# Performance work log

Hardware: AMD Instinct MI355X
Metric: run time of the kernel (lower is better)

## Reference

```python
import jax, jax.numpy as jnp
import numpy as np

B, D, H, W = 1024, 256, 8, 8
NS, ITERS, HID = 8, 5, 256  # HID = max(dim, 128)
EPS = 1e-8


def _ln(x, w, b, axes):
    mu = x.mean(axes, keepdims=True)
    var = x.var(axes, keepdims=True)
    return (x - mu) * jax.lax.rsqrt(var + 1e-5) * w + b


def _grid():
    ranges = [np.linspace(0.0, 1.0, num=r) for r in (H, W)]
    g = np.stack(np.meshgrid(*ranges, indexing='ij'), -1).reshape(H, W, -1)[None].astype(np.float32)
    return jnp.asarray(np.concatenate([g, 1.0 - g], -1))  # [1,H,W,4]


def setup_inputs():
    key = jax.random.key(0)
    ks = jax.random.split(key, 16)
    r = lambda i, shape, s=0.02: jax.random.normal(ks[i], shape, jnp.float32) * s
    d = D
    return {
        'inputs': jax.random.normal(ks[0], (B, D, H, W), jnp.float32),
        'slots_noise': jax.random.normal(ks[1], (B, NS, D), jnp.float32),
        'pos_W': r(2, (4, d)), 'pos_b': jnp.zeros((d,), jnp.float32),
        'enln_w': jnp.ones((H * W, d), jnp.float32), 'enln_b': jnp.zeros((H * W, d), jnp.float32),
        'f1W': r(3, (d, d)), 'f1b': jnp.zeros((d,), jnp.float32),
        'f2W': r(4, (d, d)), 'f2b': jnp.zeros((d,), jnp.float32),
        'ni_w': jnp.ones((d,), jnp.float32), 'ni_b': jnp.zeros((d,), jnp.float32),
        'qW': r(5, (d, d)), 'qb': jnp.zeros((d,), jnp.float32),
        'kW': r(6, (d, d)), 'kb': jnp.zeros((d,), jnp.float32),
        'vW': r(7, (d, d)), 'vb': jnp.zeros((d,), jnp.float32),
        'gih': r(8, (3 * d, d)), 'ghh': r(9, (3 * d, d)),
        'bih': jnp.zeros((3 * d,), jnp.float32), 'bhh': jnp.zeros((3 * d,), jnp.float32),
        'ns_w': jnp.ones((d,), jnp.float32), 'ns_b': jnp.zeros((d,), jnp.float32),
        'pf_w': jnp.ones((d,), jnp.float32), 'pf_b': jnp.zeros((d,), jnp.float32),
        'm1W': r(10, (d, HID)), 'm1b': jnp.zeros((HID,), jnp.float32),
        'm2W': r(11, (HID, d)), 'm2b': jnp.zeros((d,), jnp.float32),
        'slots_mu': r(12, (1, 1, d), 0.1),
        'slots_sigma': r(13, (1, 1, d), 0.1),
    }


def reference(inputs, slots_noise, pos_W, pos_b, enln_w, enln_b, f1W, f1b, f2W, f2b,
              ni_w, ni_b, qW, qb, kW, kb, vW, vb, gih, ghh, bih, bhh,
              ns_w, ns_b, pf_w, pf_b, m1W, m1b, m2W, m2b, slots_mu, slots_sigma):
    b, d = inputs.shape[0], inputs.shape[1]
    scale = d ** -0.5
    # encoder_transformation (position=True)
    x = jnp.transpose(inputs, (0, 2, 3, 1))          # [B,H,W,D]
    x = x + (_grid() @ pos_W + pos_b)                # SoftPositionEmbed
    x = x.reshape(b, H * W, d)                       # flatten spatial -> tokens
    x = _ln(x, enln_w, enln_b, (-2, -1))             # LayerNorm([ntokens, dim])
    x = jax.nn.relu(x @ f1W + f1b)
    x = jax.nn.relu(x @ f2W + f2b)
    x = _ln(x, ni_w, ni_b, (-1,))                    # norm_input
    k = x @ kW + kb                                  # [B,N,D]
    v = x @ vW + vb
    # slot init: torch.normal(mu, exp(0.5*sigma)) with explicit noise
    slots = slots_mu + jnp.exp(0.5 * slots_sigma) * slots_noise  # [B,S,D]
    for _ in range(ITERS):
        slots_prev = slots
        q = _ln(slots, ns_w, ns_b, (-1,)) @ qW + qb
        dots = jnp.einsum('bid,bjd->bij', q, k) * scale  # [B,S,N]
        attn = jax.nn.softmax(dots, axis=1) + EPS        # softmax over SLOT axis
        attn = attn / attn.sum(-1, keepdims=True)        # renormalize over tokens
        updates = jnp.einsum('bjd,bij->bid', v, attn)    # [B,S,D]
        # GRUCell(updates, slots_prev)
        gx = updates @ gih.T + bih
        gh = slots_prev @ ghh.T + bhh
        xr, xz, xn = jnp.split(gx, 3, -1)
        hr, hz, hn = jnp.split(gh, 3, -1)
        r_ = jax.nn.sigmoid(xr + hr)
        z_ = jax.nn.sigmoid(xz + hz)
        n_ = jnp.tanh(xn + r_ * hn)
        slots = (1.0 - z_) * n_ + z_ * slots_prev
        # residual MLP
        h = jax.nn.relu(_ln(slots, pf_w, pf_b, (-1,)) @ m1W + m1b)
        slots = slots + (h @ m2W + m2b)
    return slots
```

## Files before the change

kernel.cpp:

```cpp
#include <hip/hip_runtime.h>
#include <math.h>


typedef __attribute__((ext_vector_type(8))) short short8;
typedef __attribute__((ext_vector_type(4))) float f32x4;
typedef unsigned long long ull;

__device__ __forceinline__ unsigned short f2bf(float f) {
    union { float f; unsigned u; } x; x.f = f;
    unsigned r = x.u + 0x7fffu + ((x.u >> 16) & 1u);
    return (unsigned short)(r >> 16);
}
__device__ __forceinline__ float bf2f(unsigned short h) {
    union { unsigned u; float f; } x; x.u = ((unsigned)h) << 16;
    return x.f;
}
__device__ __forceinline__ float sigmoidf_(float x) { return 1.f / (1.f + expf(-x)); }
__device__ __forceinline__ ull pack4(float a, float b, float c, float d) {
    return (ull)f2bf(a) | ((ull)f2bf(b) << 16) | ((ull)f2bf(c) << 32) | ((ull)f2bf(d) << 48);
}
__device__ __forceinline__ short8 afrag256(const unsigned short* buf, int row, int k) {
    return *(const short8*)(buf + row * 256 + (k ^ ((row & 7) << 3)));
}
__device__ __forceinline__ short8 afrag64(const unsigned short* buf, int row, int k) {
// ... 201 lines not shown
                XL[lrow * 256 + ((wc + 16 + lr) ^ ((lrow & 7) << 3))] = f2bf(fmaxf(acc[mt][1][r] + b1, 0.f));
            }
    }
    __syncthreads();

    {
        const float4 w4 = *(const float4*)(niw + lane * 4);
        const float4 b4 = *(const float4*)(nib + lane * 4);
        for (int rr = 0; rr < 8; ++rr) {
            int row = wave * 8 + rr;
            ull* p = (ull*)(XL + row * 256 + ((lane * 4) ^ ((row & 7) << 3)));
            ull pk = *p;
            float v0 = bf2f((unsigned short)pk),         v1 = bf2f((unsigned short)(pk >> 16));
            float v2 = bf2f((unsigned short)(pk >> 32)), v3 = bf2f((unsigned short)(pk >> 48));
            float s1 = v0 + v1 + v2 + v3;
            float s2 = v0 * v0 + v1 * v1 + v2 * v2 + v3 * v3;
            #pragma unroll
            for (int m = 32; m >= 1; m >>= 1) { s1 += __shfl_xor(s1, m); s2 += __shfl_xor(s2, m); }
            float mu_ = s1 * (1.f / 256.f);
            float rs_ = rsqrtf(s2 * (1.f / 256.f) - mu_ * mu_ + 1e-5f);
            *p = pack4((v0 - mu_) * rs_ * w4.x + b4.x, (v1 - mu_) * rs_ * w4.y + b4.y,
                       (v2 - mu_) * rs_ * w4.z + b4.z, (v3 - mu_) * rs_ * w4.w + b4.w);
        }
    }
    __syncthreads();

    {
        short8 w0[8], w1[8];
        const unsigned short* wp0 = kt + (size_t)(wc + lr) * 256 + lk;
        const unsigned short* wp1 = kt + (size_t)(wc + 16 + lr) * 256 + lk;
        #pragma unroll
        for (int kk = 0; kk < 8; ++kk) {
            w0[kk] = *(const short8*)(wp0 + kk * 32);
            w1[kk] = *(const short8*)(wp1 + kk * 32);
        }
        const float b0 = kb[wc + lr], b1 = kb[wc + 16 + lr];
        for (int mt = 0; mt < 4; ++mt) {
            short8 a[8];
            #pragma unroll
            for (int kk = 0; kk < 8; ++kk) a[kk] = afrag256(XL, mt * 16 + lr, kk * 32 + lk);
            f32x4 a0 = (f32x4){0.f,0.f,0.f,0.f}, a1 = (f32x4){0.f,0.f,0.f,0.f};
            #pragma unroll
            for (int kk = 0; kk < 8; ++kk) {
                a0 = __builtin_amdgcn_mfma_f32_16x16x32_bf16(a[kk], w0[kk], a0, 0, 0, 0);
                a1 = __builtin_amdgcn_mfma_f32_16x16x32_bf16(a[kk], w1[kk], a1, 0, 0, 0);
            }
            #pragma unroll
            for (int r = 0; r < 4; ++r) {
                size_t row = (size_t)b * 64 + mt * 16 + mr + r;
                ks[row * 256 + wc + lr]      = f2bf(a0[r] + b0);
                ks[row * 256 + wc + 16 + lr] = f2bf(a1[r] + b1);
            }
        }
    }
    {
        short8 w0[8], w1[8];
        const unsigned short* wp0 = vwt + (size_t)(wc + lr) * 256 + lk;
        const unsigned short* wp1 = vwt + (size_t)(wc + 16 + lr) * 256 + lk;
        #pragma unroll
        for (int kk = 0; kk < 8; ++kk) {
            w0[kk] = *(const short8*)(wp0 + kk * 32);
            w1[kk] = *(const short8*)(wp1 + kk * 32);
        }
        const float b0 = vb[wc + lr], b1 = vb[wc + 16 + lr];
        for (int mt = 0; mt < 4; ++mt) {
            short8 a[8];
            #pragma unroll
            for (int kk = 0; kk < 8; ++kk) a[kk] = afrag256(XL, mt * 16 + lr, kk * 32 + lk);
            f32x4 a0 = (f32x4){0.f,0.f,0.f,0.f}, a1 = (f32x4){0.f,0.f,0.f,0.f};
            #pragma unroll
            for (int kk = 0; kk < 8; ++kk) {
                a0 = __builtin_amdgcn_mfma_f32_16x16x32_bf16(a[kk], w0[kk], a0, 0, 0, 0);
                a1 = __builtin_amdgcn_mfma_f32_16x16x32_bf16(a[kk], w1[kk], a1, 0, 0, 0);
            }
            int t0 = mt * 16 + mr;
            *(ull*)(vt + (size_t)b * 16384 + (size_t)(wc + lr) * 64 + t0) =
                pack4(a0[0] + b0, a0[1] + b0, a0[2] + b0, a0[3] + b0);
            *(ull*)(vt + (size_t)b * 16384 + (size_t)(wc + 16 + lr) * 64 + t0) =
                pack4(a1[0] + b1, a1[1] + b1, a1[2] + b1, a1[3] + b1);
        }
    }
}

__launch_bounds__(512)
__global__ void iter_kernel(
    const unsigned short* __restrict__ Kb, const unsigned short* __restrict__ Vtb,
    const unsigned short* __restrict__ qt,
    const unsigned short* __restrict__ gihb, const unsigned short* __restrict__ ghhb,
    const unsigned short* __restrict__ m1t,  const unsigned short* __restrict__ m2t,
    const float* __restrict__ qb,  const float* __restrict__ bih, const float* __restrict__ bhh,
    const float* __restrict__ pfw, const float* __restrict__ pfb,
    const float* __restrict__ m1b, const float* __restrict__ m2b,
    const float* __restrict__ nsw, const float* __restrict__ nsb,
    float* __restrict__ ping, unsigned short* __restrict__ sraw,
    unsigned short* __restrict__ lnq,
    float* __restrict__ outf, int last)
{
    __shared__ unsigned short SA[32 * 256];
    __shared__ unsigned short SS[32 * 256];
    __shared__ unsigned short QP[4][16 * 256];
    __shared__ unsigned short AT[4][16 * 64];
    __shared__ unsigned short US[32 * 256];
    __shared__ float AF[4][8][72];
    __shared__ float HL[32][256];

    const int t = threadIdx.x, lane = t & 63, wave = t >> 6;
    const int m0 = blockIdx.x * 32;
    const int b0 = blockIdx.x * 4;
    const int lr = lane & 15, lk = (lane >> 4) * 8, mr = (lane >> 4) * 4;
    const int wc = wave * 32;

    for (int i = 0; i < 4; ++i) {
        int id = t + 512 * i;
        int row = id >> 6, c4 = (id & 63) * 4;
        size_t g = ((size_t)m0 + row) * 256 + c4;
        int sw = c4 ^ ((row & 7) << 3);
        *(ull*)(SA + row * 256 + sw) = *(const ull*)(lnq + g);
        *(ull*)(SS + row * 256 + sw) = *(const ull*)(sraw + g);
    }
    for (int i = t; i < 2048; i += 512) {
        int bb = i >> 9, rem = i & 511;
        int row = 8 + (rem >> 6), c4 = (rem & 63) * 4;
        *(ull*)(&QP[bb][row * 256 + c4]) = 0;
    }
    for (int i = t; i < 1024; i += 512) ((ull*)AT)[i] = 0;
    __syncthreads();

    {
        short8 w0[8], w1[8];
        const unsigned short* wp0 = qt + (size_t)(wc + lr) * 256 + lk;
        const unsigned short* wp1 = qt + (size_t)(wc + 16 + lr) * 256 + lk;
        #pragma unroll
        for (int kk = 0; kk < 8; ++kk) {
            w0[kk] = *(const short8*)(wp0 + kk * 32);
            w1[kk] = *(const short8*)(wp1 + kk * 32);
        }
        const float bq0 = qb[wc + lr], bq1 = qb[wc + 16 + lr];
        #pragma unroll
        for (int mt = 0; mt < 2; ++mt) {
            short8 a[8];
            #pragma unroll
            for (int kk = 0; kk < 8; ++kk) a[kk] = afrag256(SA, mt * 16 + lr, kk * 32 + lk);
            f32x4 a0 = (f32x4){0.f,0.f,0.f,0.f}, a1 = (f32x4){0.f,0.f,0.f,0.f};
            #pragma unroll
            for (int kk = 0; kk < 8; ++kk) {
                a0 = __builtin_amdgcn_mfma_f32_16x16x32_bf16(a[kk], w0[kk], a0, 0, 0, 0);
                a1 = __builtin_amdgcn_mfma_f32_16x16x32_bf16(a[kk], w1[kk], a1, 0, 0, 0);
            }
            #pragma unroll
            for (int r = 0; r < 4; ++r) {
                int row = mt * 16 + mr + r;
                int bb = row >> 3, sr = row & 7;
                QP[bb][sr * 256 + ((wc + lr)      ^ (sr << 3))] = f2bf(a0[r] + bq0);
                QP[bb][sr * 256 + ((wc + 16 + lr) ^ (sr << 3))] = f2bf(a1[r] + bq1);
            }
        }
    }
    __syncthreads();

    {
        const int bb = wave >> 1, th = wave & 1;
        const int b = b0 + bb;
        short8 af[8];
        #pragma unroll
        for (int kk = 0; kk < 8; ++kk) af[kk] = afrag256(QP[bb], lr, kk * 32 + lk);
        #pragma unroll
        for (int tf = 0; tf < 2; ++tf) {
            int n0 = th * 32 + tf * 16;
            f32x4 acc = (f32x4){0.f,0.f,0.f,0.f};
            const unsigned short* kp = Kb + ((size_t)b * 64 + n0 + lr) * 256 + lk;
            #pragma unroll
            for (int kk = 0; kk < 8; ++kk)
                acc = __builtin_amdgcn_mfma_f32_16x16x32_bf16(af[kk], *(const short8*)(kp + kk * 32), acc, 0, 0, 0);
            #pragma unroll
            for (int r = 0; r < 4; ++r)
                if (mr + r < 8) AF[bb][mr + r][n0 + lr] = acc[r] * 0.0625f;
        }
    }
    __syncthreads();

    if (t < 256) {
        int b2 = t >> 6, tok = t & 63;
        float mx = AF[b2][0][tok];
        #pragma unroll
        for (int s = 1; s < 8; ++s) mx = fmaxf(mx, AF[b2][s][tok]);
        float e[8], den = 0.f;
        #pragma unroll
        for (int s = 0; s < 8; ++s) { e[s] = expf(AF[b2][s][tok] - mx); den += e[s]; }
        float inv = 1.f / den;
        #pragma unroll
        for (int s = 0; s < 8; ++s) AF[b2][s][tok] = e[s] * inv + 1e-8f;
    }
    __syncthreads();

    #pragma unroll
    for (int j = 0; j < 4; ++j) {
        int row = wave * 4 + j;
        int bb = row >> 3, sr = row & 7;
        float v = AF[bb][sr][lane];
        float ssum = v;
        #pragma unroll
        for (int m = 32; m >= 1; m >>= 1) ssum += __shfl_xor(ssum, m);
        AT[bb][sr * 64 + (lane ^ (sr << 3))] = f2bf(v / ssum);
    }
    __syncthreads();

    {
        const int bb = wave >> 1, ch = wave & 1;
        const int b = b0 + bb;
        short8 a0 = afrag64(AT[bb], lr, lk);
        short8 a1 = afrag64(AT[bb], lr, 32 + lk);
        #pragma unroll
        for (int cf = 0; cf < 8; ++cf) {
            int col = ch * 128 + cf * 16 + lr;
            const unsigned short* vp = Vtb + (size_t)b * 16384 + (size_t)col * 64;
            f32x4 acc = (f32x4){0.f,0.f,0.f,0.f};
            acc = __builtin_amdgcn_mfma_f32_16x16x32_bf16(a0, *(const short8*)(vp + lk), acc, 0, 0, 0);
            acc = __builtin_amdgcn_mfma_f32_16x16x32_bf16(a1, *(const short8*)(vp + 32 + lk), acc, 0, 0, 0);
            #pragma unroll
            for (int r = 0; r < 4; ++r)
                if (mr + r < 8) {
                    int row = bb * 8 + mr + r;
                    US[row * 256 + (col ^ ((row & 7) << 3))] = f2bf(acc[r]);
                }
        }
    }
    __syncthreads();

    {
        f32x4 aR[2][2], aZ[2][2], aN[2][2], aH[2][2];
        #pragma unroll
        for (int cf = 0; cf < 2; ++cf)
            #pragma unroll
            for (int m = 0; m < 2; ++m) {
                aR[cf][m] = (f32x4){0.f,0.f,0.f,0.f}; aZ[cf][m] = (f32x4){0.f,0.f,0.f,0.f};
                aN[cf][m] = (f32x4){0.f,0.f,0.f,0.f}; aH[cf][m] = (f32x4){0.f,0.f,0.f,0.f};
            }
        #pragma unroll
        for (int g = 0; g < 3; ++g) {
            #pragma unroll
            for (int cf = 0; cf < 2; ++cf) {
                int col = wc + cf * 16 + lr;
                const unsigned short* px = gihb + (size_t)(g * 256 + col) * 256 + lk;
                const unsigned short* ph = ghhb + (size_t)(g * 256 + col) * 256 + lk;
                short8 wx[8], wh[8];
                #pragma unroll
                for (int kk = 0; kk < 8; ++kk) {
                    wx[kk] = *(const short8*)(px + kk * 32);
                    wh[kk] = *(const short8*)(ph + kk * 32);
                }
                #pragma unroll
                for (int m = 0; m < 2; ++m) {
                    #pragma unroll
                    for (int kk = 0; kk < 8; ++kk) {
                        short8 u = afrag256(US, m * 16 + lr, kk * 32 + lk);
                        short8 s = afrag256(SS, m * 16 + lr, kk * 32 + lk);
                        if (g == 0) {
                            aR[cf][m] = __builtin_amdgcn_mfma_f32_16x16x32_bf16(u, wx[kk], aR[cf][m], 0, 0, 0);
                            aR[cf][m] = __builtin_amdgcn_mfma_f32_16x16x32_bf16(s, wh[kk], aR[cf][m], 0, 0, 0);
                        } else if (g == 1) {
                            aZ[cf][m] = __builtin_amdgcn_mfma_f32_16x16x32_bf16(u, wx[kk], aZ[cf][m], 0, 0, 0);
                            aZ[cf][m] = __builtin_amdgcn_mfma_f32_16x16x32_bf16(s, wh[kk], aZ[cf][m], 0, 0, 0);
                        } else {
                            aN[cf][m] = __builtin_amdgcn_mfma_f32_16x16x32_bf16(u, wx[kk], aN[cf][m], 0, 0, 0);
                            aH[cf][m] = __builtin_amdgcn_mfma_f32_16x16x32_bf16(s, wh[kk], aH[cf][m], 0, 0, 0);
                        }
                    }
                }
            }
        }
        #pragma unroll
        for (int cf = 0; cf < 2; ++cf) {
            int col = wc + cf * 16 + lr;
            float bR  = bih[col] + bhh[col];
            float bZ  = bih[col + 256] + bhh[col + 256];
            float bXN = bih[col + 512], bHN = bhh[col + 512];
            #pragma unroll
            for (int m = 0; m < 2; ++m)
                #pragma unroll
                for (int r = 0; r < 4; ++r) {
                    int row = m * 16 + mr + r;
                    float prev = ping[((size_t)m0 + row) * 256 + col];
                    float rr = sigmoidf_(aR[cf][m][r] + bR);
                    float zz = sigmoidf_(aZ[cf][m][r] + bZ);
                    float nn = tanhf(aN[cf][m][r] + bXN + rr * (aH[cf][m][r] + bHN));
                    HL[row][col] = (1.f - zz) * nn + zz * prev;
                }
        }
    }
    __syncthreads();
    {
        const float4 w4 = *(const float4*)(pfw + lane * 4);
        const float4 b4 = *(const float4*)(pfb + lane * 4);
        #pragma unroll
        for (int rr = 0; rr < 4; ++rr) {
            int row = wave * 4 + rr;
            float4 v = *(const float4*)&HL[row][lane * 4];
            float s1 = v.x + v.y + v.z + v.w;
            float s2 = v.x * v.x + v.y * v.y + v.z * v.z + v.w * v.w;
            #pragma unroll
            for (int m = 32; m >= 1; m >>= 1) { s1 += __shfl_xor(s1, m); s2 += __shfl_xor(s2, m); }
            float mu_ = s1 * (1.f / 256.f);
            float rs_ = rsqrtf(s2 * (1.f / 256.f) - mu_ * mu_ + 1e-5f);
            *(ull*)(SA + row * 256 + ((lane * 4) ^ ((row & 7) << 3))) = pack4(
                (v.x - mu_) * rs_ * w4.x + b4.x, (v.y - mu_) * rs_ * w4.y + b4.y,
                (v.z - mu_) * rs_ * w4.z + b4.z, (v.w - mu_) * rs_ * w4.w + b4.w);
        }
    }
    __syncthreads();

    {
        short8 w0[8], w1[8];
        const unsigned short* wp0 = m1t + (size_t)(wc + lr) * 256 + lk;
        const unsigned short* wp1 = m1t + (size_t)(wc + 16 + lr) * 256 + lk;
        #pragma unroll
        for (int kk = 0; kk < 8; ++kk) {
            w0[kk] = *(const short8*)(wp0 + kk * 32);
            w1[kk] = *(const short8*)(wp1 + kk * 32);
        }
        const float b0 = m1b[wc + lr], b1 = m1b[wc + 16 + lr];
        #pragma unroll
        for (int mt = 0; mt < 2; ++mt) {
            short8 a[8];
            #pragma unroll
            for (int kk = 0; kk < 8; ++kk) a[kk] = afrag256(SA, mt * 16 + lr, kk * 32 + lk);
            f32x4 a0 = (f32x4){0.f,0.f,0.f,0.f}, a1 = (f32x4){0.f,0.f,0.f,0.f};
            #pragma unroll
            for (int kk = 0; kk < 8; ++kk) {
                a0 = __builtin_amdgcn_mfma_f32_16x16x32_bf16(a[kk], w0[kk], a0, 0, 0, 0);
                a1 = __builtin_amdgcn_mfma_f32_16x16x32_bf16(a[kk], w1[kk], a1, 0, 0, 0);
            }
            #pragma unroll
            for (int r = 0; r < 4; ++r) {
                int row = mt * 16 + mr + r;
                US[row * 256 + ((wc + lr)      ^ ((row & 7) << 3))] = f2bf(fmaxf(a0[r] + b0, 0.f));
                US[row * 256 + ((wc + 16 + lr) ^ ((row & 7) << 3))] = f2bf(fmaxf(a1[r] + b1, 0.f));
            }
        }
    }
    __syncthreads();

    {
        short8 w0[8], w1[8];
        const unsigned short* wp0 = m2t + (size_t)(wc + lr) * 256 + lk;
        const unsigned short* wp1 = m2t + (size_t)(wc + 16 + lr) * 256 + lk;
        #pragma unroll
        for (int kk = 0; kk < 8; ++kk) {
            w0[kk] = *(const short8*)(wp0 + kk * 32);
            w1[kk] = *(const short8*)(wp1 + kk * 32);
        }
        const float b0 = m2b[wc + lr], b1 = m2b[wc + 16 + lr];
        #pragma unroll
        for (int mt = 0; mt < 2; ++mt) {
            short8 a[8];
            #pragma unroll
            for (int kk = 0; kk < 8; ++kk) a[kk] = afrag256(US, mt * 16 + lr, kk * 32 + lk);
            f32x4 a0 = (f32x4){0.f,0.f,0.f,0.f}, a1 = (f32x4){0.f,0.f,0.f,0.f};
            #pragma unroll
            for (int kk = 0; kk < 8; ++kk) {
                a0 = __builtin_amdgcn_mfma_f32_16x16x32_bf16(a[kk], w0[kk], a0, 0, 0, 0);
                a1 = __builtin_amdgcn_mfma_f32_16x16x32_bf16(a[kk], w1[kk], a1, 0, 0, 0);
            }
            #pragma unroll
            for (int r = 0; r < 4; ++r) {
                int row = mt * 16 + mr + r;
                HL[row][wc + lr]      = a0[r] + b0 + HL[row][wc + lr];
                HL[row][wc + 16 + lr] = a1[r] + b1 + HL[row][wc + 16 + lr];
            }
        }
    }
    __syncthreads();
    {
        const float4 w4 = *(const float4*)(nsw + lane * 4);
        const float4 b4 = *(const float4*)(nsb + lane * 4);
        #pragma unroll
        for (int rr = 0; rr < 4; ++rr) {
            int row = wave * 4 + rr;
            size_t off = ((size_t)m0 + row) * 256 + lane * 4;
            float4 v = *(const float4*)&HL[row][lane * 4];
            if (last) {
                *(float4*)(outf + off) = v;
            } else {
                float s1 = v.x + v.y + v.z + v.w;
                float s2 = v.x * v.x + v.y * v.y + v.z * v.z + v.w * v.w;
                #pragma unroll
                for (int m = 32; m >= 1; m >>= 1) { s1 += __shfl_xor(s1, m); s2 += __shfl_xor(s2, m); }
                float mu_ = s1 * (1.f / 256.f);
                float rs_ = rsqrtf(s2 * (1.f / 256.f) - mu_ * mu_ + 1e-5f);
                *(float4*)(ping + off) = v;
                *(ull*)(sraw + off) = pack4(v.x, v.y, v.z, v.w);
                *(ull*)(lnq + off) = pack4(
                    (v.x - mu_) * rs_ * w4.x + b4.x, (v.y - mu_) * rs_ * w4.y + b4.y,
                    (v.z - mu_) * rs_ * w4.z + b4.z, (v.w - mu_) * rs_ * w4.w + b4.w);
            }
        }
    }
}

extern "C" void kernel_launch(void* const* d_in, const int* in_sizes, int n_in,
                              void* d_out, int out_size, void* d_ws, size_t ws_size,
                              hipStream_t stream) {
    (void)in_sizes; (void)n_in; (void)ws_size; (void)out_size;
    unsigned short* wsb  = (unsigned short*)d_ws;
    unsigned short* bufB = wsb + (1u << 20);
    unsigned short* ksb  = bufB + 16777216;
    unsigned short* vtb  = ksb + 16777216;
    float* ping = (float*)(vtb + 16777216);
    unsigned short* srawb = (unsigned short*)(ping + 2097152);
    unsigned short* lnqb  = srawb + 2097152;

    const unsigned short* f1t  = wsb;
    const unsigned short* f2t  = wsb + 65536;
    const unsigned short* kt   = wsb + 131072;
    const unsigned short* vwt  = wsb + 196608;
    const unsigned short* qt   = wsb + 262144;
    const unsigned short* m1t  = wsb + 327680;
    const unsigned short* m2t  = wsb + 393216;
    const unsigned short* gihb = wsb + 458752;
    const unsigned short* ghhb = wsb + 655360;

    convert_weights<<<dim3(1664), dim3(512), 0, stream>>>(
        (const float*)d_in[6],  (const float*)d_in[8],  (const float*)d_in[14],
        (const float*)d_in[16], (const float*)d_in[12], (const float*)d_in[26],
        (const float*)d_in[28], (const float*)d_in[18], (const float*)d_in[19], wsb);

    enc1_kernel<<<dim3(1024), dim3(512), 0, stream>>>(
        (const float*)d_in[0], (const float*)d_in[2], (const float*)d_in[3],
        (const float*)d_in[4], (const float*)d_in[5],
        f1t, (const float*)d_in[7], bufB);

    enc2_kernel<<<dim3(1024), dim3(512), 0, stream>>>(
        bufB, f2t, (const float*)d_in[9],
        (const float*)d_in[10], (const float*)d_in[11],
        kt, (const float*)d_in[15], vwt, (const float*)d_in[17],
        ksb, vtb);

    slot_init<<<dim3(1024), dim3(512), 0, stream>>>(
        (const float*)d_in[30], (const float*)d_in[31], (const float*)d_in[1],
        (const float*)d_in[22], (const float*)d_in[23], ping, srawb, lnqb);

    for (int it = 0; it < 5; ++it) {
        iter_kernel<<<dim3(256), dim3(512), 0, stream>>>(
            ksb, vtb, qt, gihb, ghhb, m1t, m2t,
            (const float*)d_in[13], (const float*)d_in[20], (const float*)d_in[21],
            (const float*)d_in[24], (const float*)d_in[25],
            (const float*)d_in[27], (const float*)d_in[29],
            (const float*)d_in[22], (const float*)d_in[23],
            ping, srawb, lnqb,
            (float*)d_out, it == 4 ? 1 : 0);
    }
}
```

Before: 440.7 us.

## Double iter_kernel block size to 1024 threads, halving per-wave work

```diff
diff --git a/kernel.cpp b/kernel.cpp
--- a/kernel.cpp
+++ b/kernel.cpp
@@ -307,7 +307,7 @@
     }
 }
 
-__launch_bounds__(512)
+__launch_bounds__(1024)
 __global__ void iter_kernel(
     const unsigned short* __restrict__ Kb, const unsigned short* __restrict__ Vtb,
     const unsigned short* __restrict__ qt,
@@ -333,74 +333,64 @@
     const int m0 = blockIdx.x * 32;
     const int b0 = blockIdx.x * 4;
     const int lr = lane & 15, lk = (lane >> 4) * 8, mr = (lane >> 4) * 4;
-    const int wc = wave * 32;
-
-    for (int i = 0; i < 4; ++i) {
-        int id = t + 512 * i;
+    const int wc = wave * 16;
+
+    for (int i = 0; i < 2; ++i) {
+        int id = t + 1024 * i;
         int row = id >> 6, c4 = (id & 63) * 4;
         size_t g = ((size_t)m0 + row) * 256 + c4;
         int sw = c4 ^ ((row & 7) << 3);
         *(ull*)(SA + row * 256 + sw) = *(const ull*)(lnq + g);
         *(ull*)(SS + row * 256 + sw) = *(const ull*)(sraw + g);
     }
-    for (int i = t; i < 2048; i += 512) {
+    for (int i = t; i < 2048; i += 1024) {
         int bb = i >> 9, rem = i & 511;
         int row = 8 + (rem >> 6), c4 = (rem & 63) * 4;
         *(ull*)(&QP[bb][row * 256 + c4]) = 0;
     }
-    for (int i = t; i < 1024; i += 512) ((ull*)AT)[i] = 0;
-    __syncthreads();
-
-    {
-        short8 w0[8], w1[8];
+    if (t < 1024) ((ull*)AT)[t] = 0;
+    __syncthreads();
+
+    {
+        short8 w0[8];
         const unsigned short* wp0 = qt + (size_t)(wc + lr) * 256 + lk;
-        const unsigned short* wp1 = qt + (size_t)(wc + 16 + lr) * 256 + lk;
-        #pragma unroll
-        for (int kk = 0; kk < 8; ++kk) {
-            w0[kk] = *(const short8*)(wp0 + kk * 32);
-            w1[kk] = *(const short8*)(wp1 + kk * 32);
-        }
-        const float bq0 = qb[wc + lr], bq1 = qb[wc + 16 + lr];
+        #pragma unroll
+        for (int kk = 0; kk < 8; ++kk) w0[kk] = *(const short8*)(wp0 + kk * 32);
+        const float bq0 = qb[wc + lr];
         #pragma unroll
         for (int mt = 0; mt < 2; ++mt) {
             short8 a[8];
             #pragma unroll
             for (int kk = 0; kk < 8; ++kk) a[kk] = afrag256(SA, mt * 16 + lr, kk * 32 + lk);
-            f32x4 a0 = (f32x4){0.f,0.f,0.f,0.f}, a1 = (f32x4){0.f,0.f,0.f,0.f};
-            #pragma unroll
-            for (int kk = 0; kk < 8; ++kk) {
+            f32x4 a0 = (f32x4){0.f,0.f,0.f,0.f};
+            #pragma unroll
+            for (int kk = 0; kk < 8; ++kk)
                 a0 = __builtin_amdgcn_mfma_f32_16x16x32_bf16(a[kk], w0[kk], a0, 0, 0, 0);
-                a1 = __builtin_amdgcn_mfma_f32_16x16x32_bf16(a[kk], w1[kk], a1, 0, 0, 0);
-            }
             #pragma unroll
             for (int r = 0; r < 4; ++r) {
                 int row = mt * 16 + mr + r;
                 int bb = row >> 3, sr = row & 7;
-                QP[bb][sr * 256 + ((wc + lr)      ^ (sr << 3))] = f2bf(a0[r] + bq0);
-                QP[bb][sr * 256 + ((wc + 16 + lr) ^ (sr << 3))] = f2bf(a1[r] + bq1);
-            }
-        }
-    }
-    __syncthreads();
-
-    {
-        const int bb = wave >> 1, th = wave & 1;
+                QP[bb][sr * 256 + ((wc + lr) ^ (sr << 3))] = f2bf(a0[r] + bq0);
+            }
+        }
+    }
+    __syncthreads();
+
+    {
+        const int bb = wave >> 2, th = wave & 3;
         const int b = b0 + bb;
         short8 af[8];
         #pragma unroll
         for (int kk = 0; kk < 8; ++kk) af[kk] = afrag256(QP[bb], lr, kk * 32 + lk);
-        #pragma unroll
-        for (int tf = 0; tf < 2; ++tf) {
-            int n0 = th * 32 + tf * 16;
-            f32x4 acc = (f32x4){0.f,0.f,0.f,0.f};
-            const unsigned short* kp = Kb + ((size_t)b * 64 + n0 + lr) * 256 + lk;
-            #pragma unroll
-            for (int kk = 0; kk < 8; ++kk)
-                acc = __builtin_amdgcn_mfma_f32_16x16x32_bf16(af[kk], *(const short8*)(kp + kk * 32), acc, 0, 0, 0);
-            #pragma unroll
-            for (int r = 0; r < 4; ++r)
-                if (mr + r < 8) AF[bb][mr + r][n0 + lr] = acc[r] * 0.0625f;
-        }
+        int n0 = th * 16;
+        f32x4 acc = (f32x4){0.f,0.f,0.f,0.f};
+        const unsigned short* kp = Kb + ((size_t)b * 64 + n0 + lr) * 256 + lk;
+        #pragma unroll
+        for (int kk = 0; kk < 8; ++kk)
+            acc = __builtin_amdgcn_mfma_f32_16x16x32_bf16(af[kk], *(const short8*)(kp + kk * 32), acc, 0, 0, 0);
+        #pragma unroll
+        for (int r = 0; r < 4; ++r)
+            if (mr + r < 8) AF[bb][mr + r][n0 + lr] = acc[r] * 0.0625f;
     }
     __syncthreads();
 
@@ -419,8 +409,8 @@
     __syncthreads();
 
     #pragma unroll
-    for (int j = 0; j < 4; ++j) {
-        int row = wave * 4 + j;
+    for (int j = 0; j < 2; ++j) {
+        int row = wave * 2 + j;
         int bb = row >> 3, sr = row & 7;
         float v = AF[bb][sr][lane];
         float ssum = v;
@@ -431,13 +421,13 @@
     __syncthreads();
 
     {
-        const int bb = wave >> 1, ch = wave & 1;
+        const int bb = wave >> 2, ch = wave & 3;
         const int b = b0 + bb;
         short8 a0 = afrag64(AT[bb], lr, lk);
         short8 a1 = afrag64(AT[bb], lr, 32 + lk);
         #pragma unroll
-        for (int cf = 0; cf < 8; ++cf) {
-            int col = ch * 128 + cf * 16 + lr;
+        for (int cf = 0; cf < 4; ++cf) {
+            int col = ch * 64 + cf * 16 + lr;
             const unsigned short* vp = Vtb + (size_t)b * 16384 + (size_t)col * 64;
             f32x4 acc = (f32x4){0.f,0.f,0.f,0.f};
             acc = __builtin_amdgcn_mfma_f32_16x16x32_bf16(a0, *(const short8*)(vp + lk), acc, 0, 0, 0);
@@ -453,73 +443,64 @@
     __syncthreads();
 
     {
-        f32x4 aR[2][2], aZ[2][2], aN[2][2], aH[2][2];
-        #pragma unroll
-        for (int cf = 0; cf < 2; ++cf)
+        f32x4 aR[2], aZ[2], aN[2], aH[2];
+        #pragma unroll
+        for (int m = 0; m < 2; ++m) {
+            aR[m] = (f32x4){0.f,0.f,0.f,0.f}; aZ[m] = (f32x4){0.f,0.f,0.f,0.f};
+            aN[m] = (f32x4){0.f,0.f,0.f,0.f}; aH[m] = (f32x4){0.f,0.f,0.f,0.f};
+        }
+        const int col = wc + lr;
+        #pragma unroll
+        for (int g = 0; g < 3; ++g) {
+            const unsigned short* px = gihb + (size_t)(g * 256 + col) * 256 + lk;
+            const unsigned short* ph = ghhb + (size_t)(g * 256 + col) * 256 + lk;
+            short8 wx[8], wh[8];
+            #pragma unroll
+            for (int kk = 0; kk < 8; ++kk) {
+                wx[kk] = *(const short8*)(px + kk * 32);
+                wh[kk] = *(const short8*)(ph + kk * 32);
+            }
             #pragma unroll
             for (int m = 0; m < 2; ++m) {
-                aR[cf][m] = (f32x4){0.f,0.f,0.f,0.f}; aZ[cf][m] = (f32x4){0.f,0.f,0.f,0.f};
-                aN[cf][m] = (f32x4){0.f,0.f,0.f,0.f}; aH[cf][m] = (f32x4){0.f,0.f,0.f,0.f};
-            }
-        #pragma unroll
-        for (int g = 0; g < 3; ++g) {
-            #pragma unroll
-            for (int cf = 0; cf < 2; ++cf) {
-                int col = wc + cf * 16 + lr;
-                const unsigned short* px = gihb + (size_t)(g * 256 + col) * 256 + lk;
-                const unsigned short* ph = ghhb + (size_t)(g * 256 + col) * 256 + lk;
-                short8 wx[8], wh[8];
                 #pragma unroll
                 for (int kk = 0; kk < 8; ++kk) {
-                    wx[kk] = *(const short8*)(px + kk * 32);
-                    wh[kk] = *(const short8*)(ph + kk * 32);
-                }
-                #pragma unroll
-                for (int m = 0; m < 2; ++m) {
-                    #pragma unroll
-                    for (int kk = 0; kk < 8; ++kk) {
-                        short8 u = afrag256(US, m * 16 + lr, kk * 32 + lk);
-                        short8 s = afrag256(SS, m * 16 + lr, kk * 32 + lk);
-                        if (g == 0) {
-                            aR[cf][m] = __builtin_amdgcn_mfma_f32_16x16x32_bf16(u, wx[kk], aR[cf][m], 0, 0, 0);
-                            aR[cf][m] = __builtin_amdgcn_mfma_f32_16x16x32_bf16(s, wh[kk], aR[cf][m], 0, 0, 0);
-                        } else if (g == 1) {
-                            aZ[cf][m] = __builtin_amdgcn_mfma_f32_16x16x32_bf16(u, wx[kk], aZ[cf][m], 0, 0, 0);
-                            aZ[cf][m] = __builtin_amdgcn_mfma_f32_16x16x32_bf16(s, wh[kk], aZ[cf][m], 0, 0, 0);
-                        } else {
-                            aN[cf][m] = __builtin_amdgcn_mfma_f32_16x16x32_bf16(u, wx[kk], aN[cf][m], 0, 0, 0);
-                            aH[cf][m] = __builtin_amdgcn_mfma_f32_16x16x32_bf16(s, wh[kk], aH[cf][m], 0, 0, 0);
-                        }
+                    short8 u = afrag256(US, m * 16 + lr, kk * 32 + lk);
+                    short8 s = afrag256(SS, m * 16 + lr, kk * 32 + lk);
+                    if (g == 0) {
+                        aR[m] = __builtin_amdgcn_mfma_f32_16x16x32_bf16(u, wx[kk], aR[m], 0, 0, 0);
+                        aR[m] = __builtin_amdgcn_mfma_f32_16x16x32_bf16(s, wh[kk], aR[m], 0, 0, 0);
+                    } else if (g == 1) {
+                        aZ[m] = __builtin_amdgcn_mfma_f32_16x16x32_bf16(u, wx[kk], aZ[m], 0, 0, 0);
+                        aZ[m] = __builtin_amdgcn_mfma_f32_16x16x32_bf16(s, wh[kk], aZ[m], 0, 0, 0);
+                    } else {
+                        aN[m] = __builtin_amdgcn_mfma_f32_16x16x32_bf16(u, wx[kk], aN[m], 0, 0, 0);
+                        aH[m] = __builtin_amdgcn_mfma_f32_16x16x32_bf16(s, wh[kk], aH[m], 0, 0, 0);
                     }
                 }
             }
         }
-        #pragma unroll
-        for (int cf = 0; cf < 2; ++cf) {
-            int col = wc + cf * 16 + lr;
-            float bR  = bih[col] + bhh[col];
-            float bZ  = bih[col + 256] + bhh[col + 256];
-            float bXN = bih[col + 512], bHN = bhh[col + 512];
-            #pragma unroll
-            for (int m = 0; m < 2; ++m)
-                #pragma unroll
-                for (int r = 0; r < 4; ++r) {
-                    int row = m * 16 + mr + r;
-                    float prev = ping[((size_t)m0 + row) * 256 + col];
-                    float rr = sigmoidf_(aR[cf][m][r] + bR);
-                    float zz = sigmoidf_(aZ[cf][m][r] + bZ);
-                    float nn = tanhf(aN[cf][m][r] + bXN + rr * (aH[cf][m][r] + bHN));
-                    HL[row][col] = (1.f - zz) * nn + zz * prev;
-                }
-        }
+        float bR  = bih[col] + bhh[col];
+        float bZ  = bih[col + 256] + bhh[col + 256];
+        float bXN = bih[col + 512], bHN = bhh[col + 512];
+        #pragma unroll
+        for (int m = 0; m < 2; ++m)
+            #pragma unroll
+            for (int r = 0; r < 4; ++r) {
+                int row = m * 16 + mr + r;
+                float prev = ping[((size_t)m0 + row) * 256 + col];
+                float rr = sigmoidf_(aR[m][r] + bR);
+                float zz = sigmoidf_(aZ[m][r] + bZ);
+                float nn = tanhf(aN[m][r] + bXN + rr * (aH[m][r] + bHN));
+                HL[row][col] = (1.f - zz) * nn + zz * prev;
+            }
     }
     __syncthreads();
     {
         const float4 w4 = *(const float4*)(pfw + lane * 4);
         const float4 b4 = *(const float4*)(pfb + lane * 4);
         #pragma unroll
-        for (int rr = 0; rr < 4; ++rr) {
-            int row = wave * 4 + rr;
+        for (int rr = 0; rr < 2; ++rr) {
+            int row = wave * 2 + rr;
             float4 v = *(const float4*)&HL[row][lane * 4];
             float s1 = v.x + v.y + v.z + v.w;
             float s2 = v.x * v.x + v.y * v.y + v.z * v.z + v.w * v.w;
@@ -535,89 +516,79 @@
     __syncthreads();
 
     {
-        short8 w0[8], w1[8];
+        short8 w0[8];
         const unsigned short* wp0 = m1t + (size_t)(wc + lr) * 256 + lk;
-        const unsigned short* wp1 = m1t + (size_t)(wc + 16 + lr) * 256 + lk;
-        #pragma unroll
-        for (int kk = 0; kk < 8; ++kk) {
-            w0[kk] = *(const short8*)(wp0 + kk * 32);
-            w1[kk] = *(const short8*)(wp1 + kk * 32);
-        }
-        const float b0 = m1b[wc + lr], b1 = m1b[wc + 16 + lr];
+        #pragma unroll
+        for (int kk = 0; kk < 8; ++kk) w0[kk] = *(const short8*)(wp0 + kk * 32);
+        const float b0m = m1b[wc + lr];
         #pragma unroll
         for (int mt = 0; mt < 2; ++mt) {
             short8 a[8];
             #pragma unroll
             for (int kk = 0; kk < 8; ++kk) a[kk] = afrag256(SA, mt * 16 + lr, kk * 32 + lk);
-            f32x4 a0 = (f32x4){0.f,0.f,0.f,0.f}, a1 = (f32x4){0.f,0.f,0.f,0.f};
-            #pragma unroll
-            for (int kk = 0; kk < 8; ++kk) {
+            f32x4 a0 = (f32x4){0.f,0.f,0.f,0.f};
+            #pragma unroll
+            for (int kk = 0; kk < 8; ++kk)
                 a0 = __builtin_amdgcn_mfma_f32_16x16x32_bf16(a[kk], w0[kk], a0, 0, 0, 0);
-                a1 = __builtin_amdgcn_mfma_f32_16x16x32_bf16(a[kk], w1[kk], a1, 0, 0, 0);
-            }
             #pragma unroll
             for (int r = 0; r < 4; ++r) {
                 int row = mt * 16 + mr + r;
-                US[row * 256 + ((wc + lr)      ^ ((row & 7) << 3))] = f2bf(fmaxf(a0[r] + b0, 0.f));
-                US[row * 256 + ((wc + 16 + lr) ^ ((row & 7) << 3))] = f2bf(fmaxf(a1[r] + b1, 0.f));
-            }
-        }
-    }
-    __syncthreads();
-
-    {
-        short8 w0[8], w1[8];
+                US[row * 256 + ((wc + lr) ^ ((row & 7) << 3))] = f2bf(fmaxf(a0[r] + b0m, 0.f));
+            }
+        }
+    }
+    __syncthreads();
+
+    {
+        short8 w0[8];
         const unsigned short* wp0 = m2t + (size_t)(wc + lr) * 256 + lk;
-        const unsigned short* wp1 = m2t + (size_t)(wc + 16 + lr) * 256 + lk;
-        #pragma unroll
-        for (int kk = 0; kk < 8; ++kk) {
-            w0[kk] = *(const short8*)(wp0 + kk * 32);
-            w1[kk] = *(const short8*)(wp1 + kk * 32);
-        }
-        const float b0 = m2b[wc + lr], b1 = m2b[wc + 16 + lr];
+        #pragma unroll
+        for (int kk = 0; kk < 8; ++kk) w0[kk] = *(const short8*)(wp0 + kk * 32);
+        const float b0m = m2b[wc + lr];
         #pragma unroll
         for (int mt = 0; mt < 2; ++mt) {
             short8 a[8];
             #pragma unroll
             for (int kk = 0; kk < 8; ++kk) a[kk] = afrag256(US, mt * 16 + lr, kk * 32 + lk);
-            f32x4 a0 = (f32x4){0.f,0.f,0.f,0.f}, a1 = (f32x4){0.f,0.f,0.f,0.f};
-            #pragma unroll
-            for (int kk = 0; kk < 8; ++kk) {
+            f32x4 a0 = (f32x4){0.f,0.f,0.f,0.f};
+            #pragma unroll
+            for (int kk = 0; kk < 8; ++kk)
                 a0 = __builtin_amdgcn_mfma_f32_16x16x32_bf16(a[kk], w0[kk], a0, 0, 0, 0);
-                a1 = __builtin_amdgcn_mfma_f32_16x16x32_bf16(a[kk], w1[kk], a1, 0, 0, 0);
-            }
             #pragma unroll
             for (int r = 0; r < 4; ++r) {
                 int row = mt * 16 + mr + r;
-                HL[row][wc + lr]      = a0[r] + b0 + HL[row][wc + lr];
-                HL[row][wc + 16 + lr] = a1[r] + b1 + HL[row][wc + 16 + lr];
-            }
-        }
-    }
-    __syncthreads();
-    {
+                HL[row][wc + lr] = a0[r] + b0m + HL[row][wc + lr];
+            }
+        }
+    }
+    __syncthreads();
+
+    if (last) {
+        #pragma unroll
+        for (int rr = 0; rr < 2; ++rr) {
+            int row = wave * 2 + rr;
+            *(float4*)(outf + ((size_t)m0 + row) * 256 + lane * 4) =
+                *(const float4*)&HL[row][lane * 4];
+        }
+    } else {
         const float4 w4 = *(const float4*)(nsw + lane * 4);
         const float4 b4 = *(const float4*)(nsb + lane * 4);
         #pragma unroll
-        for (int rr = 0; rr < 4; ++rr) {
-            int row = wave * 4 + rr;
+        for (int rr = 0; rr < 2; ++rr) {
+            int row = wave * 2 + rr;
+            float4 v = *(const float4*)&HL[row][lane * 4];
+            float s1 = v.x + v.y + v.z + v.w;
+            float s2 = v.x * v.x + v.y * v.y + v.z * v.z + v.w * v.w;
+            #pragma unroll
+            for (int m = 32; m >= 1; m >>= 1) { s1 += __shfl_xor(s1, m); s2 += __shfl_xor(s2, m); }
+            float mu_ = s1 * (1.f / 256.f);
+            float rs_ = rsqrtf(s2 * (1.f / 256.f) - mu_ * mu_ + 1e-5f);
             size_t off = ((size_t)m0 + row) * 256 + lane * 4;
-            float4 v = *(const float4*)&HL[row][lane * 4];
-            if (last) {
-                *(float4*)(outf + off) = v;
-            } else {
-                float s1 = v.x + v.y + v.z + v.w;
-                float s2 = v.x * v.x + v.y * v.y + v.z * v.z + v.w * v.w;
-                #pragma unroll
-                for (int m = 32; m >= 1; m >>= 1) { s1 += __shfl_xor(s1, m); s2 += __shfl_xor(s2, m); }
-                float mu_ = s1 * (1.f / 256.f);
-                float rs_ = rsqrtf(s2 * (1.f / 256.f) - mu_ * mu_ + 1e-5f);
-                *(float4*)(ping + off) = v;
-                *(ull*)(sraw + off) = pack4(v.x, v.y, v.z, v.w);
-                *(ull*)(lnq + off) = pack4(
-                    (v.x - mu_) * rs_ * w4.x + b4.x, (v.y - mu_) * rs_ * w4.y + b4.y,
-                    (v.z - mu_) * rs_ * w4.z + b4.z, (v.w - mu_) * rs_ * w4.w + b4.w);
-            }
+            *(float4*)(ping + off) = v;
+            *(ull*)(sraw + off) = pack4(v.x, v.y, v.z, v.w);
+            *(ull*)(lnq + off) = pack4(
+                (v.x - mu_) * rs_ * w4.x + b4.x, (v.y - mu_) * rs_ * w4.y + b4.y,
+                (v.z - mu_) * rs_ * w4.z + b4.z, (v.w - mu_) * rs_ * w4.w + b4.w);
         }
     }
 }
@@ -665,7 +636,7 @@
         (const float*)d_in[22], (const float*)d_in[23], ping, srawb, lnqb);
 
     for (int it = 0; it < 5; ++it) {
-        iter_kernel<<<dim3(256), dim3(512), 0, stream>>>(
+        iter_kernel<<<dim3(256), dim3(1024), 0, stream>>>(
             ksb, vtb, qt, gihb, ghhb, m1t, m2t,
             (const float*)d_in[13], (const float*)d_in[20], (const float*)d_in[21],
             (const float*)d_in[24], (const float*)d_in[25],
```

After: 461.7 us. 4.8% more time.

## Halve per-block batch in iter_kernel to launch 512 blocks of 2 batches

Applied to the files above, without the earlier changes.

```diff
diff --git a/kernel.cpp b/kernel.cpp
--- a/kernel.cpp
+++ b/kernel.cpp
@@ -321,21 +321,21 @@
     unsigned short* __restrict__ lnq,
     float* __restrict__ outf, int last)
 {
-    __shared__ unsigned short SA[32 * 256];
-    __shared__ unsigned short SS[32 * 256];
-    __shared__ unsigned short QP[4][16 * 256];
-    __shared__ unsigned short AT[4][16 * 64];
-    __shared__ unsigned short US[32 * 256];
-    __shared__ float AF[4][8][72];
-    __shared__ float HL[32][256];
+    __shared__ unsigned short SA[16 * 256];
+    __shared__ unsigned short SS[16 * 256];
+    __shared__ unsigned short QP[2][16 * 256];
+    __shared__ unsigned short AT[2][16 * 64];
+    __shared__ unsigned short US[16 * 256];
+    __shared__ float AF[2][8][72];
+    __shared__ float HL[16][256];
 
     const int t = threadIdx.x, lane = t & 63, wave = t >> 6;
-    const int m0 = blockIdx.x * 32;
-    const int b0 = blockIdx.x * 4;
+    const int m0 = blockIdx.x * 16;
+    const int b0 = blockIdx.x * 2;
     const int lr = lane & 15, lk = (lane >> 4) * 8, mr = (lane >> 4) * 4;
     const int wc = wave * 32;
 
-    for (int i = 0; i < 4; ++i) {
+    for (int i = 0; i < 2; ++i) {
         int id = t + 512 * i;
         int row = id >> 6, c4 = (id & 63) * 4;
         size_t g = ((size_t)m0 + row) * 256 + c4;
@@ -343,12 +343,12 @@
         *(ull*)(SA + row * 256 + sw) = *(const ull*)(lnq + g);
         *(ull*)(SS + row * 256 + sw) = *(const ull*)(sraw + g);
     }
-    for (int i = t; i < 2048; i += 512) {
+    for (int i = t; i < 1024; i += 512) {
         int bb = i >> 9, rem = i & 511;
         int row = 8 + (rem >> 6), c4 = (rem & 63) * 4;
         *(ull*)(&QP[bb][row * 256 + c4]) = 0;
     }
-    for (int i = t; i < 1024; i += 512) ((ull*)AT)[i] = 0;
+    ((ull*)AT)[t] = 0;
     __syncthreads();
 
     {
@@ -361,50 +361,44 @@
             w1[kk] = *(const short8*)(wp1 + kk * 32);
         }
         const float bq0 = qb[wc + lr], bq1 = qb[wc + 16 + lr];
-        #pragma unroll
-        for (int mt = 0; mt < 2; ++mt) {
-            short8 a[8];
-            #pragma unroll
-            for (int kk = 0; kk < 8; ++kk) a[kk] = afrag256(SA, mt * 16 + lr, kk * 32 + lk);
-            f32x4 a0 = (f32x4){0.f,0.f,0.f,0.f}, a1 = (f32x4){0.f,0.f,0.f,0.f};
-            #pragma unroll
-            for (int kk = 0; kk < 8; ++kk) {
-                a0 = __builtin_amdgcn_mfma_f32_16x16x32_bf16(a[kk], w0[kk], a0, 0, 0, 0);
-                a1 = __builtin_amdgcn_mfma_f32_16x16x32_bf16(a[kk], w1[kk], a1, 0, 0, 0);
-            }
-            #pragma unroll
-            for (int r = 0; r < 4; ++r) {
-                int row = mt * 16 + mr + r;
-                int bb = row >> 3, sr = row & 7;
-                QP[bb][sr * 256 + ((wc + lr)      ^ (sr << 3))] = f2bf(a0[r] + bq0);
-                QP[bb][sr * 256 + ((wc + 16 + lr) ^ (sr << 3))] = f2bf(a1[r] + bq1);
-            }
-        }
-    }
-    __syncthreads();
-
-    {
-        const int bb = wave >> 1, th = wave & 1;
+        short8 a[8];
+        #pragma unroll
+        for (int kk = 0; kk < 8; ++kk) a[kk] = afrag256(SA, lr, kk * 32 + lk);
+        f32x4 a0 = (f32x4){0.f,0.f,0.f,0.f}, a1 = (f32x4){0.f,0.f,0.f,0.f};
+        #pragma unroll
+        for (int kk = 0; kk < 8; ++kk) {
+            a0 = __builtin_amdgcn_mfma_f32_16x16x32_bf16(a[kk], w0[kk], a0, 0, 0, 0);
+            a1 = __builtin_amdgcn_mfma_f32_16x16x32_bf16(a[kk], w1[kk], a1, 0, 0, 0);
+        }
+        #pragma unroll
+        for (int r = 0; r < 4; ++r) {
+            int row = mr + r;
+            int bb = row >> 3, sr = row & 7;
+            QP[bb][sr * 256 + ((wc + lr)      ^ (sr << 3))] = f2bf(a0[r] + bq0);
+            QP[bb][sr * 256 + ((wc + 16 + lr) ^ (sr << 3))] = f2bf(a1[r] + bq1);
+        }
+    }
+    __syncthreads();
+
+    {
+        const int bb = wave >> 2, th = wave & 3;
         const int b = b0 + bb;
         short8 af[8];
         #pragma unroll
         for (int kk = 0; kk < 8; ++kk) af[kk] = afrag256(QP[bb], lr, kk * 32 + lk);
-        #pragma unroll
-        for (int tf = 0; tf < 2; ++tf) {
-            int n0 = th * 32 + tf * 16;
-            f32x4 acc = (f32x4){0.f,0.f,0.f,0.f};
-            const unsigned short* kp = Kb + ((size_t)b * 64 + n0 + lr) * 256 + lk;
-            #pragma unroll
-            for (int kk = 0; kk < 8; ++kk)
-                acc = __builtin_amdgcn_mfma_f32_16x16x32_bf16(af[kk], *(const short8*)(kp + kk * 32), acc, 0, 0, 0);
-            #pragma unroll
-            for (int r = 0; r < 4; ++r)
-                if (mr + r < 8) AF[bb][mr + r][n0 + lr] = acc[r] * 0.0625f;
-        }
-    }
-    __syncthreads();
-
-    if (t < 256) {
+        int n0 = th * 16;
+        f32x4 acc = (f32x4){0.f,0.f,0.f,0.f};
+        const unsigned short* kp = Kb + ((size_t)b * 64 + n0 + lr) * 256 + lk;
+        #pragma unroll
+        for (int kk = 0; kk < 8; ++kk)
+            acc = __builtin_amdgcn_mfma_f32_16x16x32_bf16(af[kk], *(const short8*)(kp + kk * 32), acc, 0, 0, 0);
+        #pragma unroll
+        for (int r = 0; r < 4; ++r)
+            if (mr + r < 8) AF[bb][mr + r][n0 + lr] = acc[r] * 0.0625f;
+    }
+    __syncthreads();
+
+    if (t < 128) {
         int b2 = t >> 6, tok = t & 63;
         float mx = AF[b2][0][tok];
         #pragma unroll
@@ -419,8 +413,8 @@
     __syncthreads();
 
     #pragma unroll
-    for (int j = 0; j < 4; ++j) {
-        int row = wave * 4 + j;
+    for (int j = 0; j < 2; ++j) {
+        int row = wave * 2 + j;
         int bb = row >> 3, sr = row & 7;
         float v = AF[bb][sr][lane];
         float ssum = v;
@@ -431,13 +425,13 @@
     __syncthreads();
 
     {
-        const int bb = wave >> 1, ch = wave & 1;
+        const int bb = wave >> 2, ch = wave & 3;
         const int b = b0 + bb;
         short8 a0 = afrag64(AT[bb], lr, lk);
         short8 a1 = afrag64(AT[bb], lr, 32 + lk);
         #pragma unroll
-        for (int cf = 0; cf < 8; ++cf) {
-            int col = ch * 128 + cf * 16 + lr;
+        for (int cf = 0; cf < 4; ++cf) {
+            int col = ch * 64 + cf * 16 + lr;
             const unsigned short* vp = Vtb + (size_t)b * 16384 + (size_t)col * 64;
             f32x4 acc = (f32x4){0.f,0.f,0.f,0.f};
             acc = __builtin_amdgcn_mfma_f32_16x16x32_bf16(a0, *(const short8*)(vp + lk), acc, 0, 0, 0);
@@ -453,14 +447,18 @@
     __syncthreads();
 
     {
-        f32x4 aR[2][2], aZ[2][2], aN[2][2], aH[2][2];
-        #pragma unroll
-        for (int cf = 0; cf < 2; ++cf)
-            #pragma unroll
-            for (int m = 0; m < 2; ++m) {
-                aR[cf][m] = (f32x4){0.f,0.f,0.f,0.f}; aZ[cf][m] = (f32x4){0.f,0.f,0.f,0.f};
-                aN[cf][m] = (f32x4){0.f,0.f,0.f,0.f}; aH[cf][m] = (f32x4){0.f,0.f,0.f,0.f};
-            }
+        f32x4 aR[2], aZ[2], aN[2], aH[2];
+        #pragma unroll
+        for (int cf = 0; cf < 2; ++cf) {
+            aR[cf] = (f32x4){0.f,0.f,0.f,0.f}; aZ[cf] = (f32x4){0.f,0.f,0.f,0.f};
+            aN[cf] = (f32x4){0.f,0.f,0.f,0.f}; aH[cf] = (f32x4){0.f,0.f,0.f,0.f};
+        }
+        short8 u[8], s[8];
+        #pragma unroll
+        for (int kk = 0; kk < 8; ++kk) {
+            u[kk] = afrag256(US, lr, kk * 32 + lk);
+            s[kk] = afrag256(SS, lr, kk * 32 + lk);
+        }
         #pragma unroll
         for (int g = 0; g < 3; ++g) {
             #pragma unroll
@@ -475,21 +473,16 @@
                     wh[kk] = *(const short8*)(ph + kk * 32);
                 }
                 #pragma unroll
-                for (int m = 0; m < 2; ++m) {
-                    #pragma unroll
-                    for (int kk = 0; kk < 8; ++kk) {
-                        short8 u = afrag256(US, m * 16 + lr, kk * 32 + lk);
-                        short8 s = afrag256(SS, m * 16 + lr, kk * 32 + lk);
-                        if (g == 0) {
-                            aR[cf][m] = __builtin_amdgcn_mfma_f32_16x16x32_bf16(u, wx[kk], aR[cf][m], 0, 0, 0);
-                            aR[cf][m] = __builtin_amdgcn_mfma_f32_16x16x32_bf16(s, wh[kk], aR[cf][m], 0, 0, 0);
-                        } else if (g == 1) {
-                            aZ[cf][m] = __builtin_amdgcn_mfma_f32_16x16x32_bf16(u, wx[kk], aZ[cf][m], 0, 0, 0);
-                            aZ[cf][m] = __builtin_amdgcn_mfma_f32_16x16x32_bf16(s, wh[kk], aZ[cf][m], 0, 0, 0);
-                        } else {
-                            aN[cf][m] = __builtin_amdgcn_mfma_f32_16x16x32_bf16(u, wx[kk], aN[cf][m], 0, 0, 0);
-                            aH[cf][m] = __builtin_amdgcn_mfma_f32_16x16x32_bf16(s, wh[kk], aH[cf][m], 0, 0, 0);
-                        }
+                for (int kk = 0; kk < 8; ++kk) {
+                    if (g == 0) {
+                        aR[cf] = __builtin_amdgcn_mfma_f32_16x16x32_bf16(u[kk], wx[kk], aR[cf], 0, 0, 0);
+                        aR[cf] = __builtin_amdgcn_mfma_f32_16x16x32_bf16(s[kk], wh[kk], aR[cf], 0, 0, 0);
+                    } else if (g == 1) {
+                        aZ[cf] = __builtin_amdgcn_mfma_f32_16x16x32_bf16(u[kk], wx[kk], aZ[cf], 0, 0, 0);
+                        aZ[cf] = __builtin_amdgcn_mfma_f32_16x16x32_bf16(s[kk], wh[kk], aZ[cf], 0, 0, 0);
+                    } else {
+                        aN[cf] = __builtin_amdgcn_mfma_f32_16x16x32_bf16(u[kk], wx[kk], aN[cf], 0, 0, 0);
+                        aH[cf] = __builtin_amdgcn_mfma_f32_16x16x32_bf16(s[kk], wh[kk], aH[cf], 0, 0, 0);
                     }
                 }
             }
@@ -501,16 +494,14 @@
             float bZ  = bih[col + 256] + bhh[col + 256];
             float bXN = bih[col + 512], bHN = bhh[col + 512];
             #pragma unroll
-            for (int m = 0; m < 2; ++m)
-                #pragma unroll
-                for (int r = 0; r < 4; ++r) {
-                    int row = m * 16 + mr + r;
-                    float prev = ping[((size_t)m0 + row) * 256 + col];
-                    float rr = sigmoidf_(aR[cf][m][r] + bR);
-                    float zz = sigmoidf_(aZ[cf][m][r] + bZ);
-                    float nn = tanhf(aN[cf][m][r] + bXN + rr * (aH[cf][m][r] + bHN));
-                    HL[row][col] = (1.f - zz) * nn + zz * prev;
-                }
+            for (int r = 0; r < 4; ++r) {
+                int row = mr + r;
+                float prev = ping[((size_t)m0 + row) * 256 + col];
+                float rr = sigmoidf_(aR[cf][r] + bR);
+                float zz = sigmoidf_(aZ[cf][r] + bZ);
+                float nn = tanhf(aN[cf][r] + bXN + rr * (aH[cf][r] + bHN));
+                HL[row][col] = (1.f - zz) * nn + zz * prev;
+            }
         }
     }
     __syncthreads();
@@ -518,8 +509,8 @@
         const float4 w4 = *(const float4*)(pfw + lane * 4);
         const float4 b4 = *(const float4*)(pfb + lane * 4);
         #pragma unroll
-        for (int rr = 0; rr < 4; ++rr) {
-            int row = wave * 4 + rr;
+        for (int rr = 0; rr < 2; ++rr) {
+            int row = wave * 2 + rr;
             float4 v = *(const float4*)&HL[row][lane * 4];
             float s1 = v.x + v.y + v.z + v.w;
             float s2 = v.x * v.x + v.y * v.y + v.z * v.z + v.w * v.w;
@@ -543,24 +534,21 @@
             w0[kk] = *(const short8*)(wp0 + kk * 32);
             w1[kk] = *(const short8*)(wp1 + kk * 32);
         }
-        const float b0 = m1b[wc + lr], b1 = m1b[wc + 16 + lr];
-        #pragma unroll
-        for (int mt = 0; mt < 2; ++mt) {
-            short8 a[8];
-            #pragma unroll
-            for (int kk = 0; kk < 8; ++kk) a[kk] = afrag256(SA, mt * 16 + lr, kk * 32 + lk);
-            f32x4 a0 = (f32x4){0.f,0.f,0.f,0.f}, a1 = (f32x4){0.f,0.f,0.f,0.f};
-            #pragma unroll
-            for (int kk = 0; kk < 8; ++kk) {
-                a0 = __builtin_amdgcn_mfma_f32_16x16x32_bf16(a[kk], w0[kk], a0, 0, 0, 0);
-                a1 = __builtin_amdgcn_mfma_f32_16x16x32_bf16(a[kk], w1[kk], a1, 0, 0, 0);
-            }
-            #pragma unroll
-            for (int r = 0; r < 4; ++r) {
-                int row = mt * 16 + mr + r;
-                US[row * 256 + ((wc + lr)      ^ ((row & 7) << 3))] = f2bf(fmaxf(a0[r] + b0, 0.f));
-                US[row * 256 + ((wc + 16 + lr) ^ ((row & 7) << 3))] = f2bf(fmaxf(a1[r] + b1, 0.f));
-            }
+        const float b0m = m1b[wc + lr], b1m = m1b[wc + 16 + lr];
+        short8 a[8];
+        #pragma unroll
+        for (int kk = 0; kk < 8; ++kk) a[kk] = afrag256(SA, lr, kk * 32 + lk);
+        f32x4 a0 = (f32x4){0.f,0.f,0.f,0.f}, a1 = (f32x4){0.f,0.f,0.f,0.f};
+        #pragma unroll
+        for (int kk = 0; kk < 8; ++kk) {
+            a0 = __builtin_amdgcn_mfma_f32_16x16x32_bf16(a[kk], w0[kk], a0, 0, 0, 0);
+            a1 = __builtin_amdgcn_mfma_f32_16x16x32_bf16(a[kk], w1[kk], a1, 0, 0, 0);
+        }
+        #pragma unroll
+        for (int r = 0; r < 4; ++r) {
+            int row = mr + r;
+            US[row * 256 + ((wc + lr)      ^ ((row & 7) << 3))] = f2bf(fmaxf(a0[r] + b0m, 0.f));
+            US[row * 256 + ((wc + 16 + lr) ^ ((row & 7) << 3))] = f2bf(fmaxf(a1[r] + b1m, 0.f));
         }
     }
     __syncthreads();
@@ -574,50 +562,51 @@
             w0[kk] = *(const short8*)(wp0 + kk * 32);
             w1[kk] = *(const short8*)(wp1 + kk * 32);
         }
-        const float b0 = m2b[wc + lr], b1 = m2b[wc + 16 + lr];
-        #pragma unroll
-        for (int mt = 0; mt < 2; ++mt) {
-            short8 a[8];
-            #pragma unroll
-            for (int kk = 0; kk < 8; ++kk) a[kk] = afrag256(US, mt * 16 + lr, kk * 32 + lk);
-            f32x4 a0 = (f32x4){0.f,0.f,0.f,0.f}, a1 = (f32x4){0.f,0.f,0.f,0.f};
-            #pragma unroll
-            for (int kk = 0; kk < 8; ++kk) {
-                a0 = __builtin_amdgcn_mfma_f32_16x16x32_bf16(a[kk], w0[kk], a0, 0, 0, 0);
-                a1 = __builtin_amdgcn_mfma_f32_16x16x32_bf16(a[kk], w1[kk], a1, 0, 0, 0);
-            }
-            #pragma unroll
-            for (int r = 0; r < 4; ++r) {
-                int row = mt * 16 + mr + r;
-                HL[row][wc + lr]      = a0[r] + b0 + HL[row][wc + lr];
-                HL[row][wc + 16 + lr] = a1[r] + b1 + HL[row][wc + 16 + lr];
-            }
-        }
-    }
-    __syncthreads();
-    {
+        const float b0m = m2b[wc + lr], b1m = m2b[wc + 16 + lr];
+        short8 a[8];
+        #pragma unroll
+        for (int kk = 0; kk < 8; ++kk) a[kk] = afrag256(US, lr, kk * 32 + lk);
+        f32x4 a0 = (f32x4){0.f,0.f,0.f,0.f}, a1 = (f32x4){0.f,0.f,0.f,0.f};
+        #pragma unroll
+        for (int kk = 0; kk < 8; ++kk) {
+            a0 = __builtin_amdgcn_mfma_f32_16x16x32_bf16(a[kk], w0[kk], a0, 0, 0, 0);
+            a1 = __builtin_amdgcn_mfma_f32_16x16x32_bf16(a[kk], w1[kk], a1, 0, 0, 0);
+        }
+        #pragma unroll
+        for (int r = 0; r < 4; ++r) {
+            int row = mr + r;
+            HL[row][wc + lr]      = a0[r] + b0m + HL[row][wc + lr];
+            HL[row][wc + 16 + lr] = a1[r] + b1m + HL[row][wc + 16 + lr];
+        }
+    }
+    __syncthreads();
+
+    if (last) {
+        #pragma unroll
+        for (int rr = 0; rr < 2; ++rr) {
+            int row = wave * 2 + rr;
+            *(float4*)(outf + ((size_t)m0 + row) * 256 + lane * 4) =
+                *(const float4*)&HL[row][lane * 4];
+        }
+    } else {
         const float4 w4 = *(const float4*)(nsw + lane * 4);
         const float4 b4 = *(const float4*)(nsb + lane * 4);
         #pragma unroll
-        for (int rr = 0; rr < 4; ++rr) {
-            int row = wave * 4 + rr;
+        for (int rr = 0; rr < 2; ++rr) {
+            int row = wave * 2 + rr;
+            float4 v = *(const float4*)&HL[row][lane * 4];
+            float s1 = v.x + v.y + v.z + v.w;
+            float s2 = v.x * v.x + v.y * v.y + v.z * v.z + v.w * v.w;
+            #pragma unroll
+            for (int m = 32; m >= 1; m >>= 1) { s1 += __shfl_xor(s1, m); s2 += __shfl_xor(s2, m); }
+            float mu_ = s1 * (1.f / 256.f);
+            float rs_ = rsqrtf(s2 * (1.f / 256.f) - mu_ * mu_ + 1e-5f);
             size_t off = ((size_t)m0 + row) * 256 + lane * 4;
-            float4 v = *(const float4*)&HL[row][lane * 4];
-            if (last) {
-                *(float4*)(outf + off) = v;
-            } else {
-                float s1 = v.x + v.y + v.z + v.w;
-                float s2 = v.x * v.x + v.y * v.y + v.z * v.z + v.w * v.w;
-                #pragma unroll
-                for (int m = 32; m >= 1; m >>= 1) { s1 += __shfl_xor(s1, m); s2 += __shfl_xor(s2, m); }
-                float mu_ = s1 * (1.f / 256.f);
-                float rs_ = rsqrtf(s2 * (1.f / 256.f) - mu_ * mu_ + 1e-5f);
-                *(float4*)(ping + off) = v;
-                *(ull*)(sraw + off) = pack4(v.x, v.y, v.z, v.w);
-                *(ull*)(lnq + off) = pack4(
-                    (v.x - mu_) * rs_ * w4.x + b4.x, (v.y - mu_) * rs_ * w4.y + b4.y,
-                    (v.z - mu_) * rs_ * w4.z + b4.z, (v.w - mu_) * rs_ * w4.w + b4.w);
-            }
+            *(float4*)(ping + off) = v;
+            *(ull*)(sraw + off) = pack4(v.x, v.y, v.z, v.w);
+            *(ull*)(lnq + off) = pack4(
+                (v.x - mu_) * rs_ * w4.x + b4.x, (v.y - mu_) * rs_ * w4.y + b4.y,
+                (v.z - mu_) * rs_ * w4.z + b4.z, (v.w - mu_) * rs_ * w4.w + b4.w);
         }
     }
 }
@@ -665,7 +654,7 @@
         (const float*)d_in[22], (const float*)d_in[23], ping, srawb, lnqb);
 
     for (int it = 0; it < 5; ++it) {
-        iter_kernel<<<dim3(256), dim3(512), 0, stream>>>(
+        iter_kernel<<<dim3(512), dim3(512), 0, stream>>>(
             ksb, vtb, qt, gihb, ghhb, m1t, m2t,
             (const float*)d_in[13], (const float*)d_in[20], (const float*)d_in[21],
             (const float*)d_in[24], (const float*)d_in[25],
```

Measured after the change: 593.5 us. +34.7%, slower.
